# Performance work log

Measured on AMD Instinct MI355X. Metric: run time of the kernel, lower is better.

Reference implementation:

```python
import jax, jax.numpy as jnp
import numpy as np

N_CELLS = 100000
CHANNELS = 64
NNZ = 1600000


def _spmm(rows, cols, vals, x, n):
    # y[i] = sum_{k: rows[k]==i} vals[k] * x[cols[k]]  -- sparse Laplacian matvec over features
    return jax.ops.segment_sum(vals[:, None] * x[cols], rows, num_segments=n)


def setup_inputs() -> dict:
    key = jax.random.key(0)
    ks = jax.random.split(key, 9)
    scale = 1.0 / np.sqrt(CHANNELS)
    return {
        "x": jax.random.normal(ks[0], (N_CELLS, CHANNELS), dtype=jnp.float32),
        "down_rows": jax.random.randint(ks[1], (NNZ,), 0, N_CELLS, dtype=jnp.int32),
        "down_cols": jax.random.randint(ks[2], (NNZ,), 0, N_CELLS, dtype=jnp.int32),
        "down_vals": jax.random.normal(ks[3], (NNZ,), dtype=jnp.float32),
        "up_rows": jax.random.randint(ks[4], (NNZ,), 0, N_CELLS, dtype=jnp.int32),
        "up_cols": jax.random.randint(ks[5], (NNZ,), 0, N_CELLS, dtype=jnp.int32),
        "up_vals": jax.random.normal(ks[6], (NNZ,), dtype=jnp.float32),
        "w_conv": jax.random.normal(ks[7], (CHANNELS, CHANNELS), dtype=jnp.float32) * scale,
        "w_lin": jax.random.normal(ks[8], (CHANNELS, CHANNELS), dtype=jnp.float32) * scale,
    }


def reference(x, down_rows, down_cols, down_vals, up_rows, up_cols, up_vals, w_conv, w_lin):
    n = x.shape[0]
    xw = x @ w_conv  # shared Conv weight for both Laplacian paths
    x_down = _spmm(down_rows, down_cols, down_vals, xw, n)  # L_down @ (x W_conv)
    x_up = _spmm(up_rows, up_cols, up_vals, xw, n)          # L_up   @ (x W_conv)
    x_id = x @ w_lin                                         # bias-free Linear
    # Aggregation(update_func='sigmoid'): sum messages then activate
    return jax.nn.sigmoid(x_down + x_up + x_id)
```

## Files before the change

kernel.cpp:

```cpp
#include <hip/hip_runtime.h>
#include <hip/hip_bf16.h>
#include <hip/hip_fp16.h>

#define CH 64
#define RPB 128
#define RPB_SH 7
#define MAXNB 800
#define NGRP 8
#define SUBCAP 600
#define CAPG (NGRP * SUBCAP)
#define BATCH 3072
#define SPILLMAX 16384
#define FILL_BLOCKS 521
#define GEMM_PHYS 503
#define NVB (GEMM_PHYS * 2)

typedef __attribute__((ext_vector_type(8))) _Float16 half8;
typedef __attribute__((ext_vector_type(4))) float f32x4;

#define COLOFF_MASK 0x00FFFF80

__global__ __launch_bounds__(512) void gemm_fill_kernel(
    const float* __restrict__ x, const float* __restrict__ wc,
    const float* __restrict__ wl, __half* __restrict__ xwh,
    float* __restrict__ out, int n,
    const int* __restrict__ r1, const int* __restrict__ c1, const float* __restrict__ v1,
    const int* __restrict__ r2, const int* __restrict__ c2, const float* __restrict__ v2,
    int* __restrict__ gcur, int* __restrict__ spillcnt, int4* __restrict__ spill,
    int2* __restrict__ ebuf, int nnz, int nb) {
  __shared__ int2 stash[BATCH];
  __shared__ unsigned short sbuck[BATCH];
  __shared__ int hist[MAXNB];
  __shared__ int rbase[MAXNB];

  const int tid = threadIdx.x;

  if (blockIdx.x < (unsigned)FILL_BLOCKS) {
    const int grp = (int)(blockIdx.x & (NGRP - 1));
    const int tot = 2 * nnz;
    const int nbatches = (tot + BATCH - 1) / BATCH;
    for (int bt = blockIdx.x; bt < nbatches; bt += FILL_BLOCKS) {
      for (int i = tid; i < nb; i += 512) hist[i] = 0;
      __syncthreads();

      const int e0 = bt * BATCH;
      const int m = min(BATCH, tot - e0);
      for (int i = tid; i < m; i += 512) {
        const int e = e0 + i;
        int r, c;
        float v;
        if (e < nnz) {
          r = r1[e]; c = c1[e]; v = v1[e];
        } else {
          r = r2[e - nnz]; c = c2[e - nnz]; v = v2[e - nnz];
        }
        const int b = r >> RPB_SH;
        stash[i] = make_int2(((r & (RPB - 1)) << 24) | (c << 7), __float_as_int(v));
        sbuck[i] = (unsigned short)b;
        atomicAdd(&hist[b], 1);
      }
      __syncthreads();

      for (int b = tid; b < nb; b += 512) {
        const int c = hist[b];
        rbase[b] = c ? atomicAdd(&gcur[grp * nb + b], c) : 0;
        hist[b] = 0;
      }
      __syncthreads();

      for (int i = tid; i < m; i += 512) {
        const int b = sbuck[i];
        const int2 rec = stash[i];
        const int p = rbase[b] + atomicAdd(&hist[b], 1);
        if (p < SUBCAP) {
          ebuf[(size_t)b * CAPG + grp * SUBCAP + p] = rec;
        } else {
          const int sp = atomicAdd(spillcnt, 1);
          if (sp < SPILLMAX)
            spill[sp] = make_int4(b * RPB + (rec.x >> 24), rec.x & COLOFF_MASK,
                                  rec.y, 0);
        }
      }
      __syncthreads();
    }
    return;
  }

  const int vb = (int)(blockIdx.x - FILL_BLOCKS) * 2 + (tid >> 8);
  const int t256 = tid & 255;
  const int lane = t256 & 63;
  const int wv = t256 >> 6;
  const int mat = wv >> 1;
  const int tile = wv & 1;
  const float* __restrict__ W = mat ? wl : wc;

  const int i16 = lane & 15;
  const int kseg = lane >> 4;

  half8 bhi[4][2], blo[4][2];
#pragma unroll
  for (int nt = 0; nt < 4; ++nt)
#pragma unroll
    for (int kk = 0; kk < 2; ++kk)
#pragma unroll
      for (int j = 0; j < 8; ++j) {
        const float w = W[(kk * 32 + kseg * 8 + j) * CH + nt * 16 + i16];
        const _Float16 hh = (_Float16)w;
        bhi[nt][kk][j] = hh;
        blo[nt][kk][j] = (_Float16)(w - (float)hh);
      }

  const int ngroups = (n + 31) >> 5;
  for (int g = vb; g < ngroups; g += NVB) {
    const int base = g * 32 + tile * 16;
    const int row = base + i16;
    const int rowc = (row < n) ? row : (n - 1);
    const float* xp = x + (size_t)rowc * CH + kseg * 8;

    float af[16];
    {
      const float4 p0 = *(const float4*)(xp);
      const float4 p1 = *(const float4*)(xp + 4);
      const float4 q0 = *(const float4*)(xp + 32);
      const float4 q1 = *(const float4*)(xp + 36);
      af[0] = p0.x; af[1] = p0.y; af[2] = p0.z; af[3] = p0.w;
      af[4] = p1.x; af[5] = p1.y; af[6] = p1.z; af[7] = p1.w;
      af[8] = q0.x; af[9] = q0.y; af[10] = q0.z; af[11] = q0.w;
      af[12] = q1.x; af[13] = q1.y; af[14] = q1.z; af[15] = q1.w;
    }
    half8 ahi[2], alo[2];
#pragma unroll
    for (int kk = 0; kk < 2; ++kk)
#pragma unroll
      for (int j = 0; j < 8; ++j) {
        const float f = af[kk * 8 + j];
        const _Float16 hh = (_Float16)f;
        ahi[kk][j] = hh;
        alo[kk][j] = (_Float16)(f - (float)hh);
      }

    f32x4 acc[4];
#pragma unroll
    for (int nt = 0; nt < 4; ++nt) {
      f32x4 a = {0.f, 0.f, 0.f, 0.f};
#pragma unroll
      for (int kk = 0; kk < 2; ++kk) {
        a = __builtin_amdgcn_mfma_f32_16x16x32_f16(ahi[kk], bhi[nt][kk], a, 0, 0, 0);
        a = __builtin_amdgcn_mfma_f32_16x16x32_f16(alo[kk], bhi[nt][kk], a, 0, 0, 0);
        a = __builtin_amdgcn_mfma_f32_16x16x32_f16(ahi[kk], blo[nt][kk], a, 0, 0, 0);
      }
      acc[nt] = a;
    }

    if (mat == 0) {
#pragma unroll
      for (int nt = 0; nt < 4; ++nt)
#pragma unroll
        for (int r = 0; r < 4; ++r) {
          const int orow = base + kseg * 4 + r;
          if (orow < n)
            xwh[(size_t)orow * CH + nt * 16 + i16] = __float2half(acc[nt][r]);
        }
    } else {
#pragma unroll
      for (int nt = 0; nt < 4; ++nt)
#pragma unroll
        for (int r = 0; r < 4; ++r) {
          const int orow = base + kseg * 4 + r;
          if (orow < n)
            out[(size_t)orow * CH + nt * 16 + i16] = acc[nt][r];
        }
    }
  }
}

__global__ __launch_bounds__(512) void sortB_kernel(
    const int* __restrict__ gcur, int2* __restrict__ ebuf,
    unsigned int* __restrict__ rowinfo, int n, int nb) {
  __shared__ int2 raw[CAPG];
  __shared__ int hist[RPB];
  __shared__ int sc[RPB];
  __shared__ int cur[RPB];
  const int b = blockIdx.x;
  const int beg = b * CAPG;

  int goff[NGRP + 1];
  goff[0] = 0;
#pragma unroll
  for (int g = 0; g < NGRP; ++g) {
    const int cg = min(gcur[g * nb + b], SUBCAP);
    goff[g + 1] = goff[g] + cg;
  }
  const int cnt = goff[NGRP];

  if (threadIdx.x < RPB) hist[threadIdx.x] = 0;
  __syncthreads();

#pragma unroll
  for (int g = 0; g < NGRP; ++g) {
    const int cg = goff[g + 1] - goff[g];
    for (int i = threadIdx.x; i < cg; i += 512) {
      const int2 rec = ebuf[beg + g * SUBCAP + i];
      raw[goff[g] + i] = rec;
      atomicAdd(&hist[rec.x >> 24], 1);
    }
  }
  __syncthreads();

  int v = 0;
  if (threadIdx.x < RPB) {
    v = hist[threadIdx.x];
    sc[threadIdx.x] = v;
  }
  __syncthreads();
  for (int off = 1; off < RPB; off <<= 1) {
    int t = 0;
    if (threadIdx.x < RPB && threadIdx.x >= off) t = sc[threadIdx.x - off];
    __syncthreads();
    if (threadIdx.x < RPB) sc[threadIdx.x] += t;
    __syncthreads();
  }
  if (threadIdx.x < RPB) {
    const int ex = sc[threadIdx.x] - v;
    cur[threadIdx.x] = ex;
    const int gr = b * RPB + threadIdx.x;
    if (gr < n) rowinfo[gr] = ((unsigned int)ex << 16) | (unsigned int)v;
  }
  __syncthreads();

  for (int i = threadIdx.x; i < cnt; i += 512) {
    const int2 rec = raw[i];
    const int pos = atomicAdd(&cur[rec.x >> 24], 1);
    ebuf[beg + pos] = rec;
  }
}

union U8 {
  uint4 u4;
  __half h[8];
};

__device__ __forceinline__ void edge_fma(float* a, const U8& u, float v) {
#pragma unroll
  for (int k = 0; k < 8; ++k)
    a[k] = fmaf(v, __half2float(u.h[k]), a[k]);
}

__global__ __launch_bounds__(256) void gather_kernel(
    const unsigned int* __restrict__ rowinfo, const int2* __restrict__ ebuf,
    const char* __restrict__ xwbytes, float4* __restrict__ outf4,
    const int* __restrict__ spillcnt, const int4* __restrict__ spill,
    int n) {
  const int lane = threadIdx.x & 63;
  const int g = lane >> 3;
  const int l8 = lane & 7;
  const int l8b = l8 << 4;
  const int w = (blockIdx.x * blockDim.x + threadIdx.x) >> 6;
  const int nw = (gridDim.x * blockDim.x) >> 6;
  const int sc = min(*spillcnt, SPILLMAX);

  for (int row = w; row < n; row += nw) {
    const float4 lin0 = outf4[(size_t)row * 16 + 2 * l8];
    const float4 lin1 = outf4[(size_t)row * 16 + 2 * l8 + 1];

    float a[8];
#pragma unroll
    for (int k = 0; k < 8; ++k) a[k] = 0.f;

    const unsigned int info = rowinfo[row];
    const int beg = (row >> RPB_SH) * CAPG + (int)(info >> 16);
    const int end = beg + (int)(info & 0xFFFFu);

    int e = beg;
    for (; e + 16 <= end; e += 16) {
      const int2 rc0 = ebuf[e + g];
      const int2 rc1 = ebuf[e + 8 + g];
      U8 u0, u1;
      u0.u4 = *(const uint4*)(xwbytes + (rc0.x & COLOFF_MASK) + l8b);
      u1.u4 = *(const uint4*)(xwbytes + (rc1.x & COLOFF_MASK) + l8b);
      edge_fma(a, u0, __int_as_float(rc0.y));
      edge_fma(a, u1, __int_as_float(rc1.y));
    }
    for (; e < end; e += 8) {
      const int idx = e + g;
      const bool ok = idx < end;
      const int2 rc = ebuf[ok ? idx : (end - 1)];
      U8 u;
      u.u4 = *(const uint4*)(xwbytes + (rc.x & COLOFF_MASK) + l8b);
      edge_fma(a, u, ok ? __int_as_float(rc.y) : 0.f);
    }

    if (sc > 0) {
      for (int s = 0; s < sc; ++s) {
        const int4 r = spill[s];
        if (r.x == row && g == 0) {
          U8 u;
          u.u4 = *(const uint4*)(xwbytes + r.y + l8b);
          edge_fma(a, u, __int_as_float(r.z));
        }
      }
    }

#pragma unroll
    for (int k = 0; k < 8; ++k) {
      a[k] += __shfl_xor(a[k], 8, 64);
      a[k] += __shfl_xor(a[k], 16, 64);
      a[k] += __shfl_xor(a[k], 32, 64);
    }

    if (lane < 8) {
      float4 o0, o1;
      o0.x = 1.f / (1.f + __expf(-(lin0.x + a[0])));
      o0.y = 1.f / (1.f + __expf(-(lin0.y + a[1])));
      o0.z = 1.f / (1.f + __expf(-(lin0.z + a[2])));
      o0.w = 1.f / (1.f + __expf(-(lin0.w + a[3])));
      o1.x = 1.f / (1.f + __expf(-(lin1.x + a[4])));
      o1.y = 1.f / (1.f + __expf(-(lin1.y + a[5])));
      o1.z = 1.f / (1.f + __expf(-(lin1.z + a[6])));
      o1.w = 1.f / (1.f + __expf(-(lin1.w + a[7])));
      outf4[(size_t)row * 16 + 2 * l8] = o0;
      outf4[(size_t)row * 16 + 2 * l8 + 1] = o1;
    }
  }
}

__global__ __launch_bounds__(256) void gemm_kernel(
    const float* __restrict__ x, const float* __restrict__ wc,
    const float* __restrict__ wl, __half* __restrict__ xwh,
    float* __restrict__ out, int n) {
  const int lane = threadIdx.x & 63;
  const int wv = threadIdx.x >> 6;
  const int mat = wv >> 1;
  const int tile = wv & 1;
  const float* __restrict__ W = mat ? wl : wc;
  const int i16 = lane & 15;
  const int kseg = lane >> 4;

  half8 bhi[4][2], blo[4][2];
#pragma unroll
  for (int nt = 0; nt < 4; ++nt)
#pragma unroll
    for (int kk = 0; kk < 2; ++kk)
#pragma unroll
      for (int j = 0; j < 8; ++j) {
        const float w = W[(kk * 32 + kseg * 8 + j) * CH + nt * 16 + i16];
        const _Float16 hh = (_Float16)w;
        bhi[nt][kk][j] = hh;
        blo[nt][kk][j] = (_Float16)(w - (float)hh);
      }

  const int ngroups = (n + 31) >> 5;
  for (int g = blockIdx.x; g < ngroups; g += gridDim.x) {
    const int base = g * 32 + tile * 16;
    const int row = base + i16;
    const int rowc = (row < n) ? row : (n - 1);
    const float* xp = x + (size_t)rowc * CH + kseg * 8;
    float af[16];
    {
      const float4 p0 = *(const float4*)(xp);
      const float4 p1 = *(const float4*)(xp + 4);
      const float4 q0 = *(const float4*)(xp + 32);
      const float4 q1 = *(const float4*)(xp + 36);
      af[0] = p0.x; af[1] = p0.y; af[2] = p0.z; af[3] = p0.w;
      af[4] = p1.x; af[5] = p1.y; af[6] = p1.z; af[7] = p1.w;
      af[8] = q0.x; af[9] = q0.y; af[10] = q0.z; af[11] = q0.w;
      af[12] = q1.x; af[13] = q1.y; af[14] = q1.z; af[15] = q1.w;
    }
    half8 ahi[2], alo[2];
#pragma unroll
    for (int kk = 0; kk < 2; ++kk)
#pragma unroll
      for (int j = 0; j < 8; ++j) {
        const float f = af[kk * 8 + j];
        const _Float16 hh = (_Float16)f;
        ahi[kk][j] = hh;
        alo[kk][j] = (_Float16)(f - (float)hh);
      }
    f32x4 acc[4];
#pragma unroll
    for (int nt = 0; nt < 4; ++nt) {
      f32x4 a = {0.f, 0.f, 0.f, 0.f};
#pragma unroll
      for (int kk = 0; kk < 2; ++kk) {
        a = __builtin_amdgcn_mfma_f32_16x16x32_f16(ahi[kk], bhi[nt][kk], a, 0, 0, 0);
        a = __builtin_amdgcn_mfma_f32_16x16x32_f16(alo[kk], bhi[nt][kk], a, 0, 0, 0);
        a = __builtin_amdgcn_mfma_f32_16x16x32_f16(ahi[kk], blo[nt][kk], a, 0, 0, 0);
      }
      acc[nt] = a;
    }
    if (mat == 0) {
#pragma unroll
      for (int nt = 0; nt < 4; ++nt)
#pragma unroll
        for (int r = 0; r < 4; ++r) {
          const int orow = base + kseg * 4 + r;
          if (orow < n)
            xwh[(size_t)orow * CH + nt * 16 + i16] = __float2half(acc[nt][r]);
        }
    } else {
#pragma unroll
      for (int nt = 0; nt < 4; ++nt)
#pragma unroll
        for (int r = 0; r < 4; ++r) {
          const int orow = base + kseg * 4 + r;
          if (orow < n)
            out[(size_t)orow * CH + nt * 16 + i16] = acc[nt][r];
        }
    }
  }
}

__global__ __launch_bounds__(256) void scatter_kernel(
    const int* __restrict__ rows, const int* __restrict__ cols,
    const float* __restrict__ vals, const __half* __restrict__ xwh,
    float* __restrict__ out, int nnz) {
  const int lane = threadIdx.x & 63;
  const int wid = (blockIdx.x * blockDim.x + threadIdx.x) >> 6;
  const int nwaves = (gridDim.x * blockDim.x) >> 6;
  for (int k = wid; k < nnz; k += nwaves) {
    const float xv = __half2float(xwh[(size_t)cols[k] * CH + lane]);
    atomicAdd(&out[(size_t)rows[k] * CH + lane], vals[k] * xv);
  }
}

__global__ __launch_bounds__(256) void sigmoid_kernel(float* __restrict__ out, int n4) {
  const int i = blockIdx.x * blockDim.x + threadIdx.x;
  if (i < n4) {
    float4 v = reinterpret_cast<float4*>(out)[i];
    v.x = 1.f / (1.f + __expf(-v.x));
    v.y = 1.f / (1.f + __expf(-v.y));
    v.z = 1.f / (1.f + __expf(-v.z));
    v.w = 1.f / (1.f + __expf(-v.w));
    reinterpret_cast<float4*>(out)[i] = v;
  }
}

extern "C" void kernel_launch(void* const* d_in, const int* in_sizes, int n_in,
                              void* d_out, int out_size, void* d_ws, size_t ws_size,
                              hipStream_t stream) {
  const float* x         = (const float*)d_in[0];
  const int*   down_rows = (const int*)d_in[1];
  const int*   down_cols = (const int*)d_in[2];
  const float* down_vals = (const float*)d_in[3];
  const int*   up_rows   = (const int*)d_in[4];
  const int*   up_cols   = (const int*)d_in[5];
  const float* up_vals   = (const float*)d_in[6];
  const float* w_conv    = (const float*)d_in[7];
  const float* w_lin     = (const float*)d_in[8];

  const int n   = in_sizes[0] / CH;
  const int nnz = in_sizes[1];
  const int nb  = (n + RPB - 1) / RPB;

  float* out = (float*)d_out;

  char* p = (char*)d_ws;
  __half* xwh  = (__half*)p;  p += (size_t)n * CH * 2;
  int* gcur    = (int*)p;  p += (size_t)NGRP * nb * 4;
  int* spillc  = (int*)p;  p += 16;
  unsigned int* rowinfo = (unsigned int*)p;  p += ((size_t)n + 2) * 4;
  p = (char*)(((uintptr_t)p + 15) & ~(uintptr_t)15);
  int4* spill  = (int4*)p; p += (size_t)SPILLMAX * 16;
  int2* ebuf   = (int2*)p; p += (size_t)nb * CAPG * 8;
  const size_t need = (size_t)(p - (char*)d_ws);

  if (ws_size >= need && nb <= MAXNB && n < (1 << 17)) {
    (void)hipMemsetAsync(gcur, 0, (size_t)NGRP * nb * 4 + 16, stream);
    gemm_fill_kernel<<<FILL_BLOCKS + GEMM_PHYS, 512, 0, stream>>>(
        x, w_conv, w_lin, xwh, out, n,
        down_rows, down_cols, down_vals, up_rows, up_cols, up_vals,
        gcur, spillc, spill, ebuf, nnz, nb);
    sortB_kernel<<<nb, 512, 0, stream>>>(gcur, ebuf, rowinfo, n, nb);
    const int nblk = (n + 3) / 4;
    gather_kernel<<<nblk, 256, 0, stream>>>(rowinfo, ebuf, (const char*)xwh,
                                            (float4*)out, spillc, spill, n);
  } else {
    gemm_kernel<<<1024, 256, 0, stream>>>(x, w_conv, w_lin, xwh, out, n);
    scatter_kernel<<<4096, 256, 0, stream>>>(down_rows, down_cols, down_vals, xwh, out, nnz);
    scatter_kernel<<<4096, 256, 0, stream>>>(up_rows, up_cols, up_vals, xwh, out, nnz);
    const int n4 = (n * CH) / 4;
    sigmoid_kernel<<<(n4 + 255) / 256, 256, 0, stream>>>(out, n4);
  }
}
```

Baseline: 133.1 us.

## Fuse per-bucket sort and row gather into one kernel using LDS

Merges the bucket counting-sort kernel and the row-gather kernel into a single kernel with one block per 128-row bucket. Records are sorted straight into shared memory, and the gather then reads edge records from LDS instead of writing the sorted buffer back to global memory and rereading it. This removes a kernel launch, the rowinfo array and a global round trip of the edge buffer. In exchange there are only about 782 blocks of 512 threads, each holding roughly 38KB of LDS, so occupancy and load balance could suffer. The ebuf is now read twice from global memory, once for the histogram and once for the scatter.

```diff
diff --git a/kernel.cpp b/kernel.cpp
--- a/kernel.cpp
+++ b/kernel.cpp
@@ -174,67 +174,6 @@
   }
 }
 
-__global__ __launch_bounds__(512) void sortB_kernel(
-    const int* __restrict__ gcur, int2* __restrict__ ebuf,
-    unsigned int* __restrict__ rowinfo, int n, int nb) {
-  __shared__ int2 raw[CAPG];
-  __shared__ int hist[RPB];
-  __shared__ int sc[RPB];
-  __shared__ int cur[RPB];
-  const int b = blockIdx.x;
-  const int beg = b * CAPG;
-
-  int goff[NGRP + 1];
-  goff[0] = 0;
-#pragma unroll
-  for (int g = 0; g < NGRP; ++g) {
-    const int cg = min(gcur[g * nb + b], SUBCAP);
-    goff[g + 1] = goff[g] + cg;
-  }
-  const int cnt = goff[NGRP];
-
-  if (threadIdx.x < RPB) hist[threadIdx.x] = 0;
-  __syncthreads();
-
-#pragma unroll
-  for (int g = 0; g < NGRP; ++g) {
-    const int cg = goff[g + 1] - goff[g];
-    for (int i = threadIdx.x; i < cg; i += 512) {
-      const int2 rec = ebuf[beg + g * SUBCAP + i];
-      raw[goff[g] + i] = rec;
-      atomicAdd(&hist[rec.x >> 24], 1);
-    }
-  }
-  __syncthreads();
-
-  int v = 0;
-  if (threadIdx.x < RPB) {
-    v = hist[threadIdx.x];
-    sc[threadIdx.x] = v;
-  }
-  __syncthreads();
-  for (int off = 1; off < RPB; off <<= 1) {
-    int t = 0;
-    if (threadIdx.x < RPB && threadIdx.x >= off) t = sc[threadIdx.x - off];
-    __syncthreads();
-    if (threadIdx.x < RPB) sc[threadIdx.x] += t;
-    __syncthreads();
-  }
-  if (threadIdx.x < RPB) {
-    const int ex = sc[threadIdx.x] - v;
-    cur[threadIdx.x] = ex;
-    const int gr = b * RPB + threadIdx.x;
-    if (gr < n) rowinfo[gr] = ((unsigned int)ex << 16) | (unsigned int)v;
-  }
-  __syncthreads();
-
-  for (int i = threadIdx.x; i < cnt; i += 512) {
-    const int2 rec = raw[i];
-    const int pos = atomicAdd(&cur[rec.x >> 24], 1);
-    ebuf[beg + pos] = rec;
-  }
-}
-
 union U8 {
   uint4 u4;
   __half h[8];
@@ -246,45 +185,98 @@
     a[k] = fmaf(v, __half2float(u.h[k]), a[k]);
 }
 
-__global__ __launch_bounds__(256) void gather_kernel(
-    const unsigned int* __restrict__ rowinfo, const int2* __restrict__ ebuf,
+__global__ __launch_bounds__(512, 8) void sortgather2_kernel(
+    const int* __restrict__ gcur, const int2* __restrict__ ebuf,
     const char* __restrict__ xwbytes, float4* __restrict__ outf4,
     const int* __restrict__ spillcnt, const int4* __restrict__ spill,
-    int n) {
-  const int lane = threadIdx.x & 63;
-  const int g = lane >> 3;
+    int n, int nb) {
+  __shared__ int2 raw[CAPG];
+  __shared__ int hist[RPB];
+  __shared__ int rowstart[RPB];
+  __shared__ int cur[RPB];
+  const int tid = threadIdx.x;
+  const int b = blockIdx.x;
+  const int beg = b * CAPG;
+
+  int goff[NGRP + 1];
+  goff[0] = 0;
+#pragma unroll
+  for (int g = 0; g < NGRP; ++g)
+    goff[g + 1] = goff[g] + min(gcur[g * nb + b], SUBCAP);
+
+  if (tid < RPB) hist[tid] = 0;
+  __syncthreads();
+
+#pragma unroll
+  for (int g = 0; g < NGRP; ++g) {
+    const int cg = goff[g + 1] - goff[g];
+    for (int i = tid; i < cg; i += 512)
+      atomicAdd(&hist[ebuf[beg + g * SUBCAP + i].x >> 24], 1);
+  }
+  __syncthreads();
+
+  int v = 0;
+  if (tid < RPB) {
+    v = hist[tid];
+    cur[tid] = v;
+  }
+  __syncthreads();
+  for (int off = 1; off < RPB; off <<= 1) {
+    int t = 0;
+    if (tid < RPB && tid >= off) t = cur[tid - off];
+    __syncthreads();
+    if (tid < RPB) cur[tid] += t;
+    __syncthreads();
+  }
+  if (tid < RPB) {
+    rowstart[tid] = cur[tid] - v;
+    cur[tid] = cur[tid] - v;
+  }
+  __syncthreads();
+
+#pragma unroll
+  for (int g = 0; g < NGRP; ++g) {
+    const int cg = goff[g + 1] - goff[g];
+    for (int i = tid; i < cg; i += 512) {
+      const int2 rec = ebuf[beg + g * SUBCAP + i];
+      const int pos = atomicAdd(&cur[rec.x >> 24], 1);
+      raw[pos] = rec;
+    }
+  }
+  __syncthreads();
+
+  const int lane = tid & 63;
+  const int g8 = lane >> 3;
   const int l8 = lane & 7;
   const int l8b = l8 << 4;
-  const int w = (blockIdx.x * blockDim.x + threadIdx.x) >> 6;
-  const int nw = (gridDim.x * blockDim.x) >> 6;
+  const int wv = tid >> 6;
   const int sc = min(*spillcnt, SPILLMAX);
 
-  for (int row = w; row < n; row += nw) {
-    const float4 lin0 = outf4[(size_t)row * 16 + 2 * l8];
-    const float4 lin1 = outf4[(size_t)row * 16 + 2 * l8 + 1];
+  for (int rl = wv; rl < RPB; rl += 8) {
+    const int row = b * RPB + rl;
+    if (row >= n) continue;
 
     float a[8];
 #pragma unroll
     for (int k = 0; k < 8; ++k) a[k] = 0.f;
 
-    const unsigned int info = rowinfo[row];
-    const int beg = (row >> RPB_SH) * CAPG + (int)(info >> 16);
-    const int end = beg + (int)(info & 0xFFFFu);
-
-    int e = beg;
-    for (; e + 16 <= end; e += 16) {
-      const int2 rc0 = ebuf[e + g];
-      const int2 rc1 = ebuf[e + 8 + g];
+    const int rbeg = rowstart[rl];
+    const int rend = rbeg + hist[rl];
+
+    int e = rbeg;
+    for (; e + 16 <= rend; e += 16) {
+      const int2 rc0 = raw[e + g8];
+      const int2 rc1 = raw[e + 8 + g8];
       U8 u0, u1;
       u0.u4 = *(const uint4*)(xwbytes + (rc0.x & COLOFF_MASK) + l8b);
       u1.u4 = *(const uint4*)(xwbytes + (rc1.x & COLOFF_MASK) + l8b);
       edge_fma(a, u0, __int_as_float(rc0.y));
       edge_fma(a, u1, __int_as_float(rc1.y));
     }
-    for (; e < end; e += 8) {
-      const int idx = e + g;
-      const bool ok = idx < end;
-      const int2 rc = ebuf[ok ? idx : (end - 1)];
+    for (; e < rend; e += 8) {
+      const int idx = e + g8;
+      const bool ok = idx < rend;
+      const int2 rc = raw[ok ? idx : (rend - 1)];
       U8 u;
       u.u4 = *(const uint4*)(xwbytes + (rc.x & COLOFF_MASK) + l8b);
       edge_fma(a, u, ok ? __int_as_float(rc.y) : 0.f);
@@ -293,7 +285,7 @@
     if (sc > 0) {
       for (int s = 0; s < sc; ++s) {
         const int4 r = spill[s];
-        if (r.x == row && g == 0) {
+        if (r.x == row && g8 == 0) {
           U8 u;
           u.u4 = *(const uint4*)(xwbytes + r.y + l8b);
           edge_fma(a, u, __int_as_float(r.z));
@@ -309,6 +301,8 @@
     }
 
     if (lane < 8) {
+      const float4 lin0 = outf4[(size_t)row * 16 + 2 * l8];
+      const float4 lin1 = outf4[(size_t)row * 16 + 2 * l8 + 1];
       float4 o0, o1;
       o0.x = 1.f / (1.f + __expf(-(lin0.x + a[0])));
       o0.y = 1.f / (1.f + __expf(-(lin0.y + a[1])));
@@ -458,7 +452,6 @@
   __half* xwh  = (__half*)p;  p += (size_t)n * CH * 2;
   int* gcur    = (int*)p;  p += (size_t)NGRP * nb * 4;
   int* spillc  = (int*)p;  p += 16;
-  unsigned int* rowinfo = (unsigned int*)p;  p += ((size_t)n + 2) * 4;
   p = (char*)(((uintptr_t)p + 15) & ~(uintptr_t)15);
   int4* spill  = (int4*)p; p += (size_t)SPILLMAX * 16;
   int2* ebuf   = (int2*)p; p += (size_t)nb * CAPG * 8;
@@ -470,10 +463,8 @@
         x, w_conv, w_lin, xwh, out, n,
         down_rows, down_cols, down_vals, up_rows, up_cols, up_vals,
         gcur, spillc, spill, ebuf, nnz, nb);
-    sortB_kernel<<<nb, 512, 0, stream>>>(gcur, ebuf, rowinfo, n, nb);
-    const int nblk = (n + 3) / 4;
-    gather_kernel<<<nblk, 256, 0, stream>>>(rowinfo, ebuf, (const char*)xwh,
-                                            (float4*)out, spillc, spill, n);
+    sortgather2_kernel<<<nb, 512, 0, stream>>>(
+        gcur, ebuf, (const char*)xwh, (float4*)out, spillc, spill, n, nb);
   } else {
     gemm_kernel<<<1024, 256, 0, stream>>>(x, w_conv, w_lin, xwh, out, n);
     scatter_kernel<<<4096, 256, 0, stream>>>(down_rows, down_cols, down_vals, xwh, out, nnz);
```

Measured after the change: 127.0 us. 1.05x faster.
